# Kernel optimization log

Hardware: AMD Instinct MI355X
Metric: run time of the kernel (lower is better)

## Reference

```python
import jax, jax.numpy as jnp
import numpy as np

FP8_MAX = 448.0  # max representable magnitude of float8_e4m3fn


def _quantize_tensorwise(x):
    """Tensor-wise fp8 quantization. Returns (fp8 tensor, inverse_scale) where
    dequant = fp8.astype(f32) * inverse_scale (matches Fp8Quantization.quantize_tensorwise)."""
    amax = jnp.max(jnp.abs(x))
    inv_scale = jnp.maximum(amax / FP8_MAX, jnp.float32(1e-12))
    q = (x / inv_scale).astype(jnp.float8_e4m3fn)
    return q, inv_scale


def _fp8_mm(qa, qb, sa, sb):
    # scaled fp8 GEMM: accumulate in f32, apply product of per-tensor inverse scales
    return (qa.astype(jnp.float32) @ qb.astype(jnp.float32)) * (sa * sb)


def setup_inputs() -> dict:
    key = jax.random.key(0)
    k1, k2, k3 = jax.random.split(key, 3)
    x = jax.random.normal(k1, (4, 2048, 2048), dtype=jnp.float32)
    weight = jax.random.normal(k2, (2048, 2048), dtype=jnp.float32) * 0.02
    bias = jax.random.normal(k3, (2048,), dtype=jnp.float32) * 0.01
    return {"x": x, "weight": weight, "bias": bias}


def reference(x, weight, bias):
    # flatten leading dims: inputmat = input.view(-1, K)
    K = x.shape[-1]
    xm = x.reshape(-1, K)                      # [T, K]
    qx, sx = _quantize_tensorwise(xm)          # fp8 input + inverse scale
    qwt, swt = _quantize_tensorwise(weight.T)  # fp8 weight^T [K, N] + inverse scale
    out = _fp8_mm(qx, qwt, sx, swt) + bias     # [T, N]
    return out.reshape(*x.shape[:-1], -1)
```

## Files before the change

kernel.cpp:

```cpp
#include <hip/hip_runtime.h>
#include <stdint.h>

typedef float f32x4 __attribute__((ext_vector_type(4)));
typedef int   i32x4 __attribute__((ext_vector_type(4)));
typedef int   i32x8 __attribute__((ext_vector_type(8)));

__global__ __launch_bounds__(256) void amax2_kernel(
    const float* __restrict__ x, int nx4,
    const float* __restrict__ w, int nw4,
    int xblocks, int* __restrict__ out) {
  const float4* src;
  int n4, j0, stride, slot;
  if ((int)blockIdx.x < xblocks) {
    src = (const float4*)x; n4 = nx4; slot = 0;
    j0 = blockIdx.x * blockDim.x + threadIdx.x;
    stride = xblocks * blockDim.x;
  } else {
    src = (const float4*)w; n4 = nw4; slot = 1;
    j0 = (blockIdx.x - xblocks) * blockDim.x + threadIdx.x;
    stride = (gridDim.x - xblocks) * blockDim.x;
  }
  float m = 0.f;
  for (int j = j0; j < n4; j += stride) {
    float4 v = src[j];
    m = fmaxf(m, fmaxf(fmaxf(fabsf(v.x), fabsf(v.y)),
                       fmaxf(fabsf(v.z), fabsf(v.w))));
  }
#pragma unroll
  for (int off = 32; off; off >>= 1)
    m = fmaxf(m, __shfl_down(m, off, 64));
  __shared__ float red[4];
  const int lane = threadIdx.x & 63;
  const int wv = threadIdx.x >> 6;
  if (lane == 0) red[wv] = m;
  __syncthreads();
  if (threadIdx.x == 0) {
    m = fmaxf(fmaxf(red[0], red[1]), fmaxf(red[2], red[3]));
    atomicMax(out + slot, (int)__float_as_uint(m));
  }
}

__global__ __launch_bounds__(256) void quant2_kernel(
    const float* __restrict__ x, unsigned char* __restrict__ qx, int nx4,
    const float* __restrict__ w, unsigned char* __restrict__ qw, int nw4,
    int xblocks, const unsigned* __restrict__ amax2) {
  const float4* src;
  unsigned* dst;
  int n4, j0, stride;
  float amax;
  if ((int)blockIdx.x < xblocks) {
    src = (const float4*)x; dst = (unsigned*)qx; n4 = nx4;
    amax = __uint_as_float(amax2[0]);
    j0 = blockIdx.x * blockDim.x + threadIdx.x;
    stride = xblocks * blockDim.x;
  } else {
    src = (const float4*)w; dst = (unsigned*)qw; n4 = nw4;
    amax = __uint_as_float(amax2[1]);
    j0 = (blockIdx.x - xblocks) * blockDim.x + threadIdx.x;
    stride = (gridDim.x - xblocks) * blockDim.x;
  }
  const float inv_scale = fmaxf(amax / 448.0f, 1e-12f);
  for (int j = j0; j < n4; j += stride) {
    float4 v = src[j];
    float a0 = v.x / inv_scale;
    float a1 = v.y / inv_scale;
    float a2 = v.z / inv_scale;
    float a3 = v.w / inv_scale;
    int p = 0;
    p = __builtin_amdgcn_cvt_pk_fp8_f32(a0, a1, p, false);
    p = __builtin_amdgcn_cvt_pk_fp8_f32(a2, a3, p, true);
    dst[j] = (unsigned)p;
  }
}

#define BM 256
#define BN 256
#define BK 128
#define GEMM_LDS_BYTES (4 * 32768)

__device__ __forceinline__ void load_lds16(const void* g, void* l) {
  __builtin_amdgcn_global_load_lds(
      (const __attribute__((address_space(1))) unsigned int*)g,
      (__attribute__((address_space(3))) unsigned int*)l, 16, 0, 0);
}

__global__ __launch_bounds__(256, 1) void gemm_fp8_kernel(
    const unsigned char* __restrict__ Aq,
    const unsigned char* __restrict__ Bq,
    const float* __restrict__ bias,
    const unsigned* __restrict__ amax2,
    float* __restrict__ out,
    int T, int N, int K) {
  extern __shared__ unsigned char smem[];
  unsigned char* sA = smem;
  unsigned char* sB = smem + 65536;

  const int tid  = threadIdx.x;
  const int lane = tid & 63;
  const int wave = tid >> 6;
  const int wm = (wave >> 1) * 128;
  const int wn = (wave & 1) * 128;

  int lin = (int)(blockIdx.y * gridDim.x + blockIdx.x);
  const int nwg = (int)(gridDim.x * gridDim.y);
  if ((nwg & 7) == 0) lin = (lin & 7) * (nwg >> 3) + (lin >> 3);
  const long m0 = (long)(lin / (int)gridDim.x) * BM;
  const long n0 = (long)(lin % (int)gridDim.x) * BN;

  const long Kl = (long)K;

  const int row_s = tid >> 3;
  const int scol  = ((tid & 7) ^ (row_s & 7)) << 4;
  const int t16   = tid << 4;

  const int lm = lane & 15;
  const int qh = lane >> 4;
  const int c0 = ((qh * 2)     ^ (lm & 7)) << 4;
  const int c1 = ((qh * 2 + 1) ^ (lm & 7)) << 4;

  auto STAGE_A = [&](int Ts) {
    const unsigned char* g = Aq + (m0 + row_s) * Kl + (long)Ts * BK + scol;
    unsigned char* l = sA + ((Ts & 1) << 15) + t16;
#pragma unroll
    for (int r = 0; r < 8; ++r)
      load_lds16(g + (long)(r * 32) * Kl, l + r * 4096);
  };
  auto STAGE_B = [&](int Ts) {
    const unsigned char* g = Bq + (n0 + row_s) * Kl + (long)Ts * BK + scol;
    unsigned char* l = sB + ((Ts & 1) << 15) + t16;
#pragma unroll
    for (int r = 0; r < 8; ++r)
      load_lds16(g + (long)(r * 32) * Kl, l + r * 4096);
  };
  auto LDA = [&](const unsigned char* base, int mt) {
    const unsigned char* p = base + (wm + mt * 16 + lm) * BK;
    i32x4 lo = *(const i32x4*)(p + c0);
    i32x4 hi = *(const i32x4*)(p + c1);
    return (i32x8){lo.x, lo.y, lo.z, lo.w, hi.x, hi.y, hi.z, hi.w};
  };
  auto LDB = [&](const unsigned char* base, int nt) {
    const unsigned char* p = base + (wn + nt * 16 + lm) * BK;
    i32x4 lo = *(const i32x4*)(p + c0);
    i32x4 hi = *(const i32x4*)(p + c1);
    return (i32x8){lo.x, lo.y, lo.z, lo.w, hi.x, hi.y, hi.z, hi.w};
  };

  f32x4 acc[8][8];
#pragma unroll
  for (int i = 0; i < 8; ++i)
#pragma unroll
    for (int j = 0; j < 8; ++j) acc[i][j] = (f32x4){0.f, 0.f, 0.f, 0.f};

  const int nt = K / BK;

  STAGE_A(0); STAGE_B(0);
  asm volatile("s_waitcnt vmcnt(0)" ::: "memory");
  __builtin_amdgcn_s_barrier();
  __builtin_amdgcn_sched_barrier(0);

  i32x8 af[8], bf[8];
  for (int t = 0; t < nt; ++t) {
    const unsigned char* a = sA + ((t & 1) << 15);
    const unsigned char* b = sB + ((t & 1) << 15);

    if (t + 1 < nt) { STAGE_A(t + 1); STAGE_B(t + 1); }
    __builtin_amdgcn_sched_barrier(0);

    af[0] = LDA(a, 0);
#pragma unroll
    for (int j = 0; j < 8; ++j) bf[j] = LDB(b, j);
#pragma unroll
    for (int i = 1; i < 8; ++i) af[i] = LDA(a, i);

#pragma unroll
    for (int i = 0; i < 8; ++i)
#pragma unroll
      for (int j = 0; j < 8; ++j)
        acc[i][j] = __builtin_amdgcn_mfma_scale_f32_16x16x128_f8f6f4(
            af[i], bf[j], acc[i][j], 0, 0, 0, 0x7f7f7f7f, 0, 0x7f7f7f7f);

    asm volatile("s_waitcnt vmcnt(0)" ::: "memory");
    __builtin_amdgcn_s_barrier();
    __builtin_amdgcn_sched_barrier(0);
  }

  const float fsx = fmaxf(__uint_as_float(amax2[0]) / 448.0f, 1e-12f);
  const float fsw = fmaxf(__uint_as_float(amax2[1]) / 448.0f, 1e-12f);
  const float scale = fsx * fsw;
  const int rbase = qh * 4;
  float bv[8];
#pragma unroll
  for (int j = 0; j < 8; ++j) bv[j] = bias[n0 + wn + j * 16 + lm];
#pragma unroll
  for (int mt = 0; mt < 8; ++mt) {
#pragma unroll
    for (int r = 0; r < 4; ++r) {
      const long row = m0 + wm + mt * 16 + rbase + r;
      float* orow = out + row * (long)N + n0 + wn;
#pragma unroll
      for (int j = 0; j < 8; ++j)
        orow[j * 16 + lm] = acc[mt][j][r] * scale + bv[j];
    }
  }
}

extern "C" void kernel_launch(void* const* d_in, const int* in_sizes, int n_in,
                              void* d_out, int out_size, void* d_ws, size_t ws_size,
                              hipStream_t stream) {
  const float* x = (const float*)d_in[0];
  const float* w = (const float*)d_in[1];
  const float* bias = (const float*)d_in[2];
  float* out = (float*)d_out;

  const int N = in_sizes[2];
  const int K = in_sizes[1] / N;
  const int T = in_sizes[0] / K;

  unsigned* amax2 = (unsigned*)d_ws;
  unsigned char* qx = (unsigned char*)d_ws + 256;
  unsigned char* qw = qx + (size_t)T * K;

  const int XB = 1024;
  const int WB = 256;
  amax2_kernel<<<XB + WB, 256, 0, stream>>>(x, T * K / 4, w, N * K / 4, XB,
                                            (int*)amax2);
  quant2_kernel<<<XB + WB, 256, 0, stream>>>(x, qx, T * K / 4, w, qw, N * K / 4,
                                             XB, amax2);

  static bool lds_attr_set = false;
  if (!lds_attr_set) {
    (void)hipFuncSetAttribute((const void*)gemm_fp8_kernel,
                              hipFuncAttributeMaxDynamicSharedMemorySize,
                              GEMM_LDS_BYTES);
    lds_attr_set = true;
  }
  dim3 grid(N / BN, T / BM);
  gemm_fp8_kernel<<<grid, 256, GEMM_LDS_BYTES, stream>>>(qx, qw, bias, amax2,
                                                         out, T, N, K);
}
```

Measured before the change: 187.2 us.

## Prefetch next-tile B fragments into registers mid-compute with ping-pong buffers

```diff
diff --git a/kernel.cpp b/kernel.cpp
--- a/kernel.cpp
+++ b/kernel.cpp
@@ -136,13 +136,13 @@
     const unsigned char* p = base + (wm + mt * 16 + lm) * BK;
     i32x4 lo = *(const i32x4*)(p + c0);
     i32x4 hi = *(const i32x4*)(p + c1);
-    return (i32x8){lo.x, lo.y, lo.z, lo.w, hi.x, hi.y, hi.z, hi.w};
+    return __builtin_shufflevector(lo, hi, 0, 1, 2, 3, 4, 5, 6, 7);
   };
   auto LDB = [&](const unsigned char* base, int nt) {
     const unsigned char* p = base + (wn + nt * 16 + lm) * BK;
     i32x4 lo = *(const i32x4*)(p + c0);
     i32x4 hi = *(const i32x4*)(p + c1);
-    return (i32x8){lo.x, lo.y, lo.z, lo.w, hi.x, hi.y, hi.z, hi.w};
+    return __builtin_shufflevector(lo, hi, 0, 1, 2, 3, 4, 5, 6, 7);
   };
 
   f32x4 acc[8][8];
@@ -152,37 +152,63 @@
     for (int j = 0; j < 8; ++j) acc[i][j] = (f32x4){0.f, 0.f, 0.f, 0.f};
 
   const int nt = K / BK;
+
+#define SB __builtin_amdgcn_sched_barrier(0)
+#define MM(AF, BF, CI, CJ)                                               \
+  acc[CI][CJ] = __builtin_amdgcn_mfma_scale_f32_16x16x128_f8f6f4(        \
+      AF, BF[CJ], acc[CI][CJ], 0, 0, 0, 0x7f7f7f7f, 0, 0x7f7f7f7f)
+#define MBLOCK(R, AX, AY, BF)                                            \
+  _Pragma("unroll")                                                      \
+  for (int j = 0; j < 8; ++j) { MM(AX, BF, R, j); MM(AY, BF, (R) + 1, j); }
+
+#define TILE_BODY(PA, PBN, BFC, BFN, T)                                  \
+  {                                                                      \
+    if ((T) + 1 < nt) { STAGE_A((T) + 1); STAGE_B((T) + 1); }            \
+    SB;                                                                  \
+    i32x8 af0 = LDA(PA, 0), af1 = LDA(PA, 1), af2 = LDA(PA, 2),          \
+          af3 = LDA(PA, 3), af4 = LDA(PA, 4), af5 = LDA(PA, 5),          \
+          af6 = LDA(PA, 6), af7 = LDA(PA, 7);                            \
+    SB;                                                                  \
+    MBLOCK(0, af0, af1, BFC);                                            \
+    SB;                                                                  \
+    MBLOCK(2, af2, af3, BFC);                                            \
+    SB;                                                                  \
+    MBLOCK(4, af4, af5, BFC);                                            \
+    SB;                                                                  \
+    asm volatile("s_waitcnt vmcnt(0)" ::: "memory");                     \
+    __builtin_amdgcn_s_barrier();                                        \
+    SB;                                                                  \
+    if ((T) + 1 < nt) {                                                  \
+      _Pragma("unroll")                                                  \
+      for (int j = 0; j < 8; ++j) BFN[j] = LDB(PBN, j);                  \
+    }                                                                    \
+    SB;                                                                  \
+    MBLOCK(6, af6, af7, BFC);                                            \
+    SB;                                                                  \
+  }
+
+  const unsigned char* a0 = sA;
+  const unsigned char* a1 = sA + 32768;
+  const unsigned char* b0 = sB;
+  const unsigned char* b1 = sB + 32768;
 
   STAGE_A(0); STAGE_B(0);
   asm volatile("s_waitcnt vmcnt(0)" ::: "memory");
   __builtin_amdgcn_s_barrier();
-  __builtin_amdgcn_sched_barrier(0);
-
-  i32x8 af[8], bf[8];
-  for (int t = 0; t < nt; ++t) {
-    const unsigned char* a = sA + ((t & 1) << 15);
-    const unsigned char* b = sB + ((t & 1) << 15);
-
-    if (t + 1 < nt) { STAGE_A(t + 1); STAGE_B(t + 1); }
-    __builtin_amdgcn_sched_barrier(0);
-
-    af[0] = LDA(a, 0);
-#pragma unroll
-    for (int j = 0; j < 8; ++j) bf[j] = LDB(b, j);
-#pragma unroll
-    for (int i = 1; i < 8; ++i) af[i] = LDA(a, i);
-
-#pragma unroll
-    for (int i = 0; i < 8; ++i)
-#pragma unroll
-      for (int j = 0; j < 8; ++j)
-        acc[i][j] = __builtin_amdgcn_mfma_scale_f32_16x16x128_f8f6f4(
-            af[i], bf[j], acc[i][j], 0, 0, 0, 0x7f7f7f7f, 0, 0x7f7f7f7f);
-
-    asm volatile("s_waitcnt vmcnt(0)" ::: "memory");
-    __builtin_amdgcn_s_barrier();
-    __builtin_amdgcn_sched_barrier(0);
-  }
+  SB;
+  i32x8 bfE[8], bfO[8];
+#pragma unroll
+  for (int j = 0; j < 8; ++j) bfE[j] = LDB(b0, j);
+  SB;
+
+  for (int t = 0; t < nt; t += 2) {
+    TILE_BODY(a0, b1, bfE, bfO, t);
+    TILE_BODY(a1, b0, bfO, bfE, t + 1);
+  }
+#undef TILE_BODY
+#undef MBLOCK
+#undef MM
+#undef SB
 
   const float fsx = fmaxf(__uint_as_float(amax2[0]) / 448.0f, 1e-12f);
   const float fsw = fmaxf(__uint_as_float(amax2[1]) / 448.0f, 1e-12f);
```

Measured after the change: 304.4 us. 62.6% more time.
